# Optimization experiments

Hardware: AMD Instinct MI355X
Metric: run time of the kernel (lower is better)

Reference implementation:

```python
import jax, jax.numpy as jnp
import numpy as np

B, C, H, W = 4, 512, 128, 128
CI = C // 2   # inter_planes
CQ = C // 8   # q/k dim in CrossAttention


def conv1x1(x, w, b=None):
    # x: [B,Cin,H,W], w: [Cout,Cin]
    y = jnp.einsum('oc,bchw->bohw', w, x)
    if b is not None:
        y = y + b[None, :, None, None]
    return y


def setup_inputs() -> dict:
    key = jax.random.key(0)
    ks = jax.random.split(key, 13)
    s = 0.05
    return {
        'x': jax.random.normal(ks[0], (B, C, H, W), jnp.float32),
        # SCCA gating params (1x1 convs, no bias except conv_up)
        'w_q_right': jax.random.normal(ks[1], (1, C), jnp.float32) * s,
        'w_v_right': jax.random.normal(ks[2], (CI, C), jnp.float32) * s,
        'w_up': jax.random.normal(ks[3], (C, CI), jnp.float32) * s,
        'b_up': jnp.zeros((C,), jnp.float32),
        'w_q_left': jax.random.normal(ks[4], (CI, C), jnp.float32) * s,
        'w_v_left': jax.random.normal(ks[5], (CI, C), jnp.float32) * s,
        # CrossAttention params (1x1 convs with bias)
        'wq': jax.random.normal(ks[6], (CQ, C), jnp.float32) * s,
        'bq': jnp.zeros((CQ,), jnp.float32),
        'wk': jax.random.normal(ks[7], (CQ, C), jnp.float32) * s,
        'bk': jnp.zeros((CQ,), jnp.float32),
        'wv': jax.random.normal(ks[8], (C, C), jnp.float32) * s,
        'bv': jnp.zeros((C,), jnp.float32),
        'gamma': jnp.asarray(0.5, jnp.float32),
    }


def cross_attention(x, wq, bq, wk, bk, wv, bv, gamma):
    # criss-cross attention: each pixel attends to its row and column
    b, c, h, w = x.shape
    q = conv1x1(x, wq, bq)   # [B,CQ,H,W]
    k = conv1x1(x, wk, bk)   # [B,CQ,H,W]
    v = conv1x1(x, wv, bv)   # [B,C,H,W]
    # column (H) affinities with -inf on the self diagonal (as in INF())
    diag = jnp.where(jnp.eye(h, dtype=bool), -jnp.inf, 0.0).astype(x.dtype)
    e_h = jnp.einsum('bchw,bcgw->bhwg', q, k) + diag[None, :, None, :]  # [B,H,W,H]
    e_w = jnp.einsum('bchw,bchv->bhwv', q, k)                            # [B,H,W,W]
    att = jax.nn.softmax(jnp.concatenate([e_h, e_w], axis=-1), axis=-1)  # [B,H,W,H+W]
    a_h, a_w = att[..., :h], att[..., h:]
    out_h = jnp.einsum('bcgw,bhwg->bchw', v, a_h)
    out_w = jnp.einsum('bchv,bhwv->bchw', v, a_w)
    return gamma * (out_h + out_w) + x


def spatial_weighted(x, w_q_right, w_v_right, w_up, b_up):
    b, c, h, w = x.shape
    input_x = conv1x1(x, w_v_right).reshape(b, CI, h * w)       # [B,CI,HW]
    mask = jax.nn.softmax(conv1x1(x, w_q_right).reshape(b, h * w), axis=-1)  # [B,HW]
    ctx = jnp.einsum('bcn,bn->bc', input_x, mask)               # [B,CI]
    ctx = jnp.einsum('oc,bc->bo', w_up, ctx) + b_up             # [B,C]
    mask_ch = jax.nn.sigmoid(ctx)[:, :, None, None]
    return x * mask_ch


def channel_weighted(x, w_q_left, w_v_left):
    b, c, h, w = x.shape
    g_x = conv1x1(x, w_q_left)                                  # [B,CI,H,W]
    avg = g_x.mean(axis=(2, 3))                                 # [B,CI]
    theta = conv1x1(x, w_v_left).reshape(b, CI, h * w)          # [B,CI,HW]
    ctx = jax.nn.softmax(jnp.einsum('bc,bcn->bn', avg, theta), axis=-1)
    mask_sp = jax.nn.sigmoid(ctx).reshape(b, 1, h, w)
    return x * mask_sp


def reference(x, w_q_right, w_v_right, w_up, b_up, w_q_left, w_v_left,
              wq, bq, wk, bk, wv, bv, gamma):
    cc = spatial_weighted(x, w_q_right, w_v_right, w_up, b_up)
    cc = cross_attention(cc, wq, bq, wk, bk, wv, bv, gamma)
    cs = channel_weighted(x, w_q_left, w_v_left)
    cs = cross_attention(cs, wq, bq, wk, bk, wv, bv, gamma)
    out = cs + cc
    out = cross_attention(out, wq, bq, wk, bk, wv, bv, gamma)
    return out
```

## Files before the change

kernel.cpp:

```cpp
#include <hip/hip_runtime.h>
#include <hip/hip_bf16.h>
#include <math.h>

typedef __hip_bfloat16 bf16;
typedef __attribute__((ext_vector_type(8))) short s16x8;
typedef __attribute__((ext_vector_type(4))) float f32x4;

constexpr int Bn  = 4;
constexpr int Cn  = 512;
constexpr int Hn  = 128;
constexpr int Wn  = 128;
constexpr int Nn  = Hn * Wn;
constexpr int CQn = 64;
constexpr int CIn = 256;

__device__ __forceinline__ float bf2f(bf16 v){ return __bfloat162float(v); }
__device__ __forceinline__ bf16  f2bf(float v){ return __float2bfloat16(v); }

__device__ __forceinline__ void gload_lds16(const void* g, void* l){
  __builtin_amdgcn_global_load_lds(
      (const __attribute__((address_space(1))) unsigned int*)g,
      (__attribute__((address_space(3))) unsigned int*)l,
      16, 0, 0);
}


__global__ __launch_bounds__(256) void k_dotc(const float* __restrict__ x,
                                              const float* __restrict__ w,
                                              int wstride,
                                              float* __restrict__ out){
  int t = blockIdx.x * 256 + threadIdx.x;
  int b = t >> 14;
  const float* wp = w + (size_t)b * wstride;
  const float* xp = x + (size_t)b * Cn * Nn + (t & (Nn - 1));
  float acc = 0.f;
  #pragma unroll 8
  for (int c = 0; c < Cn; ++c) acc += wp[c] * xp[(size_t)c * Nn];
  out[t] = acc;
}

__global__ __launch_bounds__(256) void k_rowmean(const float* __restrict__ x,
                                                 float* __restrict__ out,
                                                 float scale){
  int bc = blockIdx.x;
  const float* xp = x + (size_t)bc * Nn;
  float acc = 0.f;
  for (int n = threadIdx.x; n < Nn; n += 256) acc += xp[n];
  for (int o = 32; o > 0; o >>= 1) acc += __shfl_down(acc, o);
  __shared__ float red[4];
  if ((threadIdx.x & 63) == 0) red[threadIdx.x >> 6] = acc;
  __syncthreads();
  if (threadIdx.x == 0) out[bc] = (red[0] + red[1] + red[2] + red[3]) * scale;
}

__global__ __launch_bounds__(256) void k_rowdot(const float* __restrict__ W,
                                                const float* __restrict__ vec,
                                                float* __restrict__ out){
  __shared__ float vs[Cn];
  int b = blockIdx.x, t = threadIdx.x;
  for (int j = t; j < Cn; j += 256) vs[j] = vec[b * Cn + j];
  __syncthreads();
  const float4* wp = (const float4*)(W + (size_t)t * Cn);
  float a = 0.f;
  #pragma unroll 4
  for (int j = 0; j < Cn / 4; ++j){
    float4 w4 = wp[j];
    a += w4.x * vs[4*j] + w4.y * vs[4*j+1] + w4.z * vs[4*j+2] + w4.w * vs[4*j+3];
  }
  out[b * CIn + t] = a;
}

__global__ __launch_bounds__(256) void k_coldot(const float* __restrict__ W,
                                                const float* __restrict__ vec,
                                                float* __restrict__ out){
  __shared__ float vs[CIn];
  int b = blockIdx.y, t = threadIdx.x;
  int c = blockIdx.x * 256 + t;
  if (t < CIn) vs[t] = vec[b * CIn + t];
  __syncthreads();
  float a = 0.f;
  #pragma unroll 8
  for (int j = 0; j < CIn; ++j) a += W[(size_t)j * Cn + c] * vs[j];
  out[b * Cn + c] = a;
}

__global__ __launch_bounds__(256) void k_mch2(const float* __restrict__ w_up,
                                              const float* __restrict__ b_up,
                                              const float* __restrict__ ctx,
                                              float* __restrict__ mch){
  __shared__ float cs[CIn];
  int b = blockIdx.y, t = threadIdx.x;
  int o = blockIdx.x * 256 + t;
  if (t < CIn) cs[t] = ctx[b * CIn + t];
  __syncthreads();
  const float4* wp = (const float4*)(w_up + (size_t)o * CIn);
  float a = b_up[o];
  #pragma unroll 4
  for (int j = 0; j < CIn / 4; ++j){
    float4 w4 = wp[j];
    a += w4.x * cs[4*j] + w4.y * cs[4*j+1] + w4.z * cs[4*j+2] + w4.w * cs[4*j+3];
  }
  mch[b * Cn + o] = 1.f / (1.f + expf(-a));
}

__global__ __launch_bounds__(1024) void k_stats(const float* __restrict__ vv,
                                                float* __restrict__ stats){
  int b = blockIdx.x;
  const float* pp = vv + (size_t)b * Nn;
  int t = threadIdx.x;
  float m = -3.4e38f;
  for (int n = t; n < Nn; n += 1024) m = fmaxf(m, pp[n]);
  for (int o = 32; o > 0; o >>= 1) m = fmaxf(m, __shfl_down(m, o));
  __shared__ float red[16];
  int wid = t >> 6, lid = t & 63;
  if (lid == 0) red[wid] = m;
  __syncthreads();
  if (t == 0){
    float q = red[0];
    for (int i = 1; i < 16; i++) q = fmaxf(q, red[i]);
    red[0] = q;
  }
  __syncthreads();
  m = red[0];
  __syncthreads();
  float s = 0.f;
  for (int n = t; n < Nn; n += 1024) s += expf(pp[n] - m);
  for (int o = 32; o > 0; o >>= 1) s += __shfl_down(s, o);
  if (lid == 0) red[wid] = s;
  __syncthreads();
  if (t == 0){
    float q = 0.f;
    for (int i = 0; i < 16; i++) q += red[i];
    stats[b * 2]     = m;
    stats[b * 2 + 1] = q;
  }
}

__global__ __launch_bounds__(256) void k_weighted(const float* __restrict__ x,
                                                  const float* __restrict__ logits,
                                                  const float* __restrict__ stats,
                                                  float* __restrict__ out){
  int bc = blockIdx.x;
  int b = bc >> 9;
  const float* xp = x + (size_t)bc * Nn;
  const float* lp = logits + (size_t)b * Nn;
  float m = stats[b * 2], den = stats[b * 2 + 1];
  float acc = 0.f;
  for (int n = threadIdx.x; n < Nn; n += 256) acc += xp[n] * expf(lp[n] - m);
  for (int o = 32; o > 0; o >>= 1) acc += __shfl_down(acc, o);
  __shared__ float red[4];
  if ((threadIdx.x & 63) == 0) red[threadIdx.x >> 6] = acc;
  __syncthreads();
  if (threadIdx.x == 0) out[bc] = (red[0] + red[1] + red[2] + red[3]) / den;
}

__global__ __launch_bounds__(256) void k_msp(const float* __restrict__ lg,
                                             const float* __restrict__ stats,
                                             float* __restrict__ msp){
  int t = blockIdx.x * 256 + threadIdx.x;
  int b = t >> 14;
  float v = expf(lg[t] - stats[b * 2]) / stats[b * 2 + 1];
  msp[t] = 1.f / (1.f + expf(-v));
}

__global__ __launch_bounds__(256) void k_applyT3(const float* __restrict__ x,
                                                 const float* __restrict__ mch,
                                                 const float* __restrict__ msp,
                                                 bf16* __restrict__ cc_hi,
                                                 bf16* __restrict__ cc_lo,
                                                 bf16* __restrict__ cs_hi,
                                                 bf16* __restrict__ cs_lo){
  __shared__ bf16 tch[32][33], tcl[32][33], tsh[32][33], tsl[32][33];
  int nt = blockIdx.x, ct = blockIdx.y, b = blockIdx.z;
  int n0 = nt * 32, c0 = ct * 32;
  int t = threadIdx.x;
  #pragma unroll
  for (int kk = 0; kk < 4; ++kk){
    int idx = t + kk * 256;
    int cl = idx >> 5, nl = idx & 31;
    float xv = x[((size_t)(b * Cn + c0 + cl)) * Nn + n0 + nl];
    float ccv = xv * mch[b * Cn + c0 + cl];
    float csv = xv * msp[b * Nn + n0 + nl];
    bf16 h1 = f2bf(ccv);
    tch[cl][nl] = h1;
    tcl[cl][nl] = f2bf(ccv - bf2f(h1));
    bf16 h2 = f2bf(csv);
    tsh[cl][nl] = h2;
    tsl[cl][nl] = f2bf(csv - bf2f(h2));
  }
  __syncthreads();
  #pragma unroll
  for (int kk = 0; kk < 4; ++kk){
    int idx = t + kk * 256;
    int nl = idx >> 5, cl = idx & 31;
    size_t o = ((size_t)(b * Nn + n0 + nl)) * Cn + c0 + cl;
    cc_hi[o] = tch[cl][nl];
    cc_lo[o] = tcl[cl][nl];
    cs_hi[o] = tsh[cl][nl];
    cs_lo[o] = tsl[cl][nl];
  }
}


__global__ __launch_bounds__(256) void k_cvt_w(const float* __restrict__ in,
                                               bf16* __restrict__ out, int n){
  int t = blockIdx.x * 256 + threadIdx.x;
  if (t < n) out[t] = f2bf(in[t]);
}

__global__ __launch_bounds__(256) void k_prep_wqk(const float* __restrict__ wq,
                                                  const float* __restrict__ wk,
                                                  const float* __restrict__ bq,
                                                  const float* __restrict__ bk,
                                                  bf16* __restrict__ wqk_hi,
                                                  bf16* __restrict__ wqk_lo,
                                                  float* __restrict__ bqk){
  int t = blockIdx.x * 256 + threadIdx.x;
  int o = t >> 9, c = t & 511;
  float v = (o < 64) ? wq[(size_t)o * Cn + c] : wk[(size_t)(o - 64) * Cn + c];
  bf16 h = f2bf(v);
  wqk_hi[t] = h;
  wqk_lo[t] = f2bf(v - bf2f(h));
  if (t < 128) bqk[t] = (t < 64) ? bq[t] : bk[t - 64];
}

__global__ __launch_bounds__(256) void k_cvt_T(const float* __restrict__ in,
                                               bf16* __restrict__ out_hi,
                                               bf16* __restrict__ out_lo){
  __shared__ bf16 th_[32][33];
  __shared__ bf16 tl_[32][33];
  int nt = blockIdx.x, ct = blockIdx.y, b = blockIdx.z;
  int n0 = nt * 32, c0 = ct * 32;
  int t = threadIdx.x;
  #pragma unroll
  for (int kk = 0; kk < 4; ++kk){
    int idx = t + kk * 256;
    int cl = idx >> 5, nl = idx & 31;
    float v = in[((size_t)(b * Cn + c0 + cl)) * Nn + n0 + nl];
    bf16 h = f2bf(v);
    th_[cl][nl] = h;
    tl_[cl][nl] = f2bf(v - bf2f(h));
  }
  __syncthreads();
  #pragma unroll
  for (int kk = 0; kk < 4; ++kk){
    int idx = t + kk * 256;
    int nl = idx >> 5, cl = idx & 31;
    size_t o = ((size_t)(b * Nn + n0 + nl)) * Cn + c0 + cl;
    out_hi[o] = th_[cl][nl];
    out_lo[o] = tl_[cl][nl];
  }
}


__global__ __launch_bounds__(256) void k_v_mfma(const bf16* __restrict__ xT,
                                                const bf16* __restrict__ wvb,
                                                const float* __restrict__ bv,
                                                bf16* __restrict__ v){
  __shared__ short As[128 * 64];
  __shared__ short Bs[128 * 64];
  __shared__ float bvs[128];
  int lin = blockIdx.x;
  int swz = (lin & 7) * 256 + (lin >> 3);
  int cb = (swz & 3) * 128;
  int nb = ((swz >> 2) & 127) * 128;
  int b  = swz >> 9;
  int t = threadIdx.x, lane = t & 63, wid = t >> 6;
  int wm = wid >> 1, wn = wid & 1;
  int l15 = lane & 15, l4 = lane >> 4;
  if (t < 128) bvs[t] = bv[cb + t];
  f32x4 acc[4][4];
  #pragma unroll
  for (int i = 0; i < 4; i++)
    #pragma unroll
    for (int j = 0; j < 4; j++) acc[i][j] = (f32x4){0.f, 0.f, 0.f, 0.f};

  const bf16* wp = wvb + (size_t)cb * Cn;
  const bf16* xp = xT + ((size_t)b * Nn + nb) * Cn;
  int r8 = lane >> 3;
  int kc = (lane & 7) * 8;
  for (int kt = 0; kt < 8; ++kt){
    int k0 = kt * 64;
    #pragma unroll
    for (int j = 0; j < 4; ++j){
      int inst = wid * 4 + j;
      int row = inst * 8 + r8;
      gload_lds16(wp + (size_t)row * Cn + k0 + kc, (char*)As + inst * 1024);
      gload_lds16(xp + (size_t)row * Cn + k0 + kc, (char*)Bs + inst * 1024);
    }
    __syncthreads();
    #pragma unroll
    for (int kk = 0; kk < 64; kk += 32){
      s16x8 a[4], bb[4];
      #pragma unroll
      for (int mi = 0; mi < 4; mi++)
        a[mi] = *(const s16x8*)&As[(wm * 64 + mi * 16 + l15) * 64 + kk + l4 * 8];
      #pragma unroll
      for (int ni = 0; ni < 4; ni++)
        bb[ni] = *(const s16x8*)&Bs[(wn * 64 + ni * 16 + l15) * 64 + kk + l4 * 8];
      #pragma unroll
      for (int mi = 0; mi < 4; mi++)
        #pragma unroll
        for (int ni = 0; ni < 4; ni++)
          acc[mi][ni] = __builtin_amdgcn_mfma_f32_16x16x32_bf16(a[mi], bb[ni], acc[mi][ni], 0, 0, 0);
    }
    __syncthreads();
  }
  #pragma unroll
  for (int mi = 0; mi < 4; mi++){
    #pragma unroll
    for (int r = 0; r < 4; r++){
      int cl = wm * 64 + mi * 16 + l4 * 4 + r;
      int c  = cb + cl;
      float bias = bvs[cl];
      #pragma unroll
      for (int ni = 0; ni < 4; ni++){
        int n = nb + wn * 64 + ni * 16 + l15;
        v[((size_t)(b * Cn + c)) * Nn + n] = f2bf(acc[mi][ni][r] + bias);
      }
    }
  }
}

__global__ __launch_bounds__(256) void k_qk_mfma(const bf16* __restrict__ xT_hi,
                                                 const bf16* __restrict__ xT_lo,
                                                 const bf16* __restrict__ wqk_hi,
                                                 const bf16* __restrict__ wqk_lo,
                                                 const float* __restrict__ bqk,
                                                 bf16* __restrict__ qhw,
                                                 bf16* __restrict__ khw){
  __shared__ char smem[65536];
  short* Ah = (short*)smem;
  short* Al = Ah + 8192;
  short* Bh = Al + 8192;
  short* Bl = Bh + 8192;
  char*  Os = smem;
  __shared__ float bs[128];
  int h = blockIdx.x, b = blockIdx.y;
  int nb = h * 128;
  int t = threadIdx.x, lane = t & 63, wid = t >> 6;
  int wm = wid >> 1, wn = wid & 1;
  int l15 = lane & 15, l4 = lane >> 4;
  if (t < 128) bs[t] = bqk[t];
  f32x4 acc[4][4];
  #pragma unroll
  for (int i = 0; i < 4; i++)
    #pragma unroll
    for (int j = 0; j < 4; j++) acc[i][j] = (f32x4){0.f, 0.f, 0.f, 0.f};

  const bf16* xh = xT_hi + ((size_t)b * Nn + nb) * Cn;
  const bf16* xl = xT_lo + ((size_t)b * Nn + nb) * Cn;
  int r8 = lane >> 3;
  int kc = (lane & 7) * 8;
  for (int kt = 0; kt < 8; ++kt){
    int k0 = kt * 64;
    #pragma unroll
    for (int j = 0; j < 4; ++j){
      int inst = wid * 4 + j;
      int row = inst * 8 + r8;
      size_t off = (size_t)row * Cn + k0 + kc;
      gload_lds16(wqk_hi + off, (char*)Ah + inst * 1024);
      gload_lds16(wqk_lo + off, (char*)Al + inst * 1024);
      gload_lds16(xh + off,     (char*)Bh + inst * 1024);
      gload_lds16(xl + off,     (char*)Bl + inst * 1024);
    }
    __syncthreads();
    #pragma unroll
    for (int kk = 0; kk < 64; kk += 32){
      s16x8 ah[4], al[4], bh[4], bl[4];
      #pragma unroll
      for (int mi = 0; mi < 4; mi++){
        int idx = (wm * 64 + mi * 16 + l15) * 64 + kk + l4 * 8;
        ah[mi] = *(const s16x8*)&Ah[idx];
        al[mi] = *(const s16x8*)&Al[idx];
      }
      #pragma unroll
      for (int ni = 0; ni < 4; ni++){
        int idx = (wn * 64 + ni * 16 + l15) * 64 + kk + l4 * 8;
        bh[ni] = *(const s16x8*)&Bh[idx];
        bl[ni] = *(const s16x8*)&Bl[idx];
      }
      #pragma unroll
      for (int mi = 0; mi < 4; mi++)
        #pragma unroll
        for (int ni = 0; ni < 4; ni++){
          acc[mi][ni] = __builtin_amdgcn_mfma_f32_16x16x32_bf16(ah[mi], bh[ni], acc[mi][ni], 0, 0, 0);
          acc[mi][ni] = __builtin_amdgcn_mfma_f32_16x16x32_bf16(ah[mi], bl[ni], acc[mi][ni], 0, 0, 0);
          acc[mi][ni] = __builtin_amdgcn_mfma_f32_16x16x32_bf16(al[mi], bh[ni], acc[mi][ni], 0, 0, 0);
        }
    }
    __syncthreads();
  }
  #pragma unroll
  for (int mi = 0; mi < 4; mi++){
    #pragma unroll
    for (int r = 0; r < 4; r++){
      int o = wm * 64 + mi * 16 + l4 * 4 + r;
      float bias = bs[o];
      #pragma unroll
      for (int ni = 0; ni < 4; ni++){
        int n = wn * 64 + ni * 16 + l15;
        bf16 bv = f2bf(acc[mi][ni][r] + bias);
        int byte = (n * 256 + o * 2) ^ ((n & 7) << 4);
        *(unsigned short*)(Os + byte) = *(unsigned short*)&bv;
      }
    }
  }
  __syncthreads();
  #pragma unroll
  for (int i = 0; i < 8; ++i){
    int s = t + i * 256;
    int row = s >> 3, seg = s & 7;
    int w = row & 127, qk = row >> 7;
    int o0 = qk * 64 + seg * 8;
    int byte = (w * 256 + o0 * 2) ^ ((w & 7) << 4);
    s16x8 d = *(const s16x8*)(Os + byte);
    bf16* dst = (qk == 0 ? qhw : khw) + (((size_t)b * Wn + w) * Hn + h) * CQn + seg * 8;
    *(s16x8*)dst = d;
  }
}


__global__ __launch_bounds__(256) void k_att_h(const bf16* __restrict__ qhw,
                                               const bf16* __restrict__ khw,
                                               const bf16* __restrict__ vT,
                                               float* __restrict__ mh,
                                               float* __restrict__ sh,
                                               bf16* __restrict__ ohX){
  __shared__ char smem[65536];
  char* attb = smem;
  char* vbb  = smem + 32768;
  float* redm = (float*)(smem + 32768);
  float* reds = redm + 256;
  int w = blockIdx.x, b = blockIdx.y;
  int t = threadIdx.x, lane = t & 63, wid = t >> 6;
  int wm = wid >> 1, wn = wid & 1;
  int l15 = lane & 15, l4 = lane >> 4;

  const bf16* qp = qhw + ((size_t)(b * Wn + w)) * (Hn * CQn);
  const bf16* kp = khw + ((size_t)(b * Wn + w)) * (Hn * CQn);
  f32x4 acc[4][4];
  #pragma unroll
  for (int i = 0; i < 4; i++)
    #pragma unroll
    for (int j = 0; j < 4; j++) acc[i][j] = (f32x4){0.f, 0.f, 0.f, 0.f};
  #pragma unroll
  for (int kk = 0; kk < 64; kk += 32){
    s16x8 a[4], bb[4];
    #pragma unroll
    for (int mi = 0; mi < 4; mi++)
      a[mi] = *(const s16x8*)(qp + (size_t)(wm * 64 + mi * 16 + l15) * CQn + kk + l4 * 8);
    #pragma unroll
    for (int ni = 0; ni < 4; ni++)
      bb[ni] = *(const s16x8*)(kp + (size_t)(wn * 64 + ni * 16 + l15) * CQn + kk + l4 * 8);
    #pragma unroll
    for (int mi = 0; mi < 4; mi++)
      #pragma unroll
      for (int ni = 0; ni < 4; ni++)
        acc[mi][ni] = __builtin_amdgcn_mfma_f32_16x16x32_bf16(a[mi], bb[ni], acc[mi][ni], 0, 0, 0);
  }
  if (wm == wn){
    #pragma unroll
    for (int mi = 0; mi < 4; mi++)
      #pragma unroll
      for (int r = 0; r < 4; r++)
        if (l15 == l4 * 4 + r) acc[mi][mi][r] = -1e30f;
  }
  float rm[4][4];
  #pragma unroll
  for (int mi = 0; mi < 4; mi++)
    #pragma unroll
    for (int r = 0; r < 4; r++){
      float m = fmaxf(fmaxf(acc[mi][0][r], acc[mi][1][r]),
                      fmaxf(acc[mi][2][r], acc[mi][3][r]));
      m = fmaxf(m, __shfl_xor(m, 1));
      m = fmaxf(m, __shfl_xor(m, 2));
      m = fmaxf(m, __shfl_xor(m, 4));
      m = fmaxf(m, __shfl_xor(m, 8));
      rm[mi][r] = m;
    }
  if (l15 == 0){
    #pragma unroll
    for (int mi = 0; mi < 4; mi++)
      #pragma unroll
      for (int r = 0; r < 4; r++)
        redm[wn * 128 + wm * 64 + mi * 16 + l4 * 4 + r] = rm[mi][r];
  }
  __syncthreads();
  float rs[4][4];
  #pragma unroll
  for (int mi = 0; mi < 4; mi++)
    #pragma unroll
    for (int r = 0; r < 4; r++){
      int h = wm * 64 + mi * 16 + l4 * 4 + r;
      float m = fmaxf(redm[h], redm[128 + h]);
      rm[mi][r] = m;
      float s = 0.f;
      #pragma unroll
      for (int ni = 0; ni < 4; ni++){
        acc[mi][ni][r] = expf(acc[mi][ni][r] - m);
        s += acc[mi][ni][r];
      }
      s += __shfl_xor(s, 1);
      s += __shfl_xor(s, 2);
      s += __shfl_xor(s, 4);
      s += __shfl_xor(s, 8);
      rs[mi][r] = s;
    }
  if (l15 == 0){
    #pragma unroll
    for (int mi = 0; mi < 4; mi++)
      #pragma unroll
      for (int r = 0; r < 4; r++)
        reds[wn * 128 + wm * 64 + mi * 16 + l4 * 4 + r] = rs[mi][r];
  }
  __syncthreads();
  #pragma unroll
  for (int mi = 0; mi < 4; mi++)
    #pragma unroll
    for (int r = 0; r < 4; r++){
      int h = wm * 64 + mi * 16 + l4 * 4 + r;
      if (wn == 0 && l15 == 0){
        mh[(size_t)(b * Wn + w) * Hn + h] = rm[mi][r];
        sh[(size_t)(b * Wn + w) * Hn + h] = reds[h] + reds[128 + h];
      }
      #pragma unroll
      for (int ni = 0; ni < 4; ni++){
        int g = wn * 64 + ni * 16 + l15;
        bf16 bv = f2bf(acc[mi][ni][r]);
        int byte = (h * 256 + g * 2) ^ ((h & 7) << 4);
        *(unsigned short*)(attb + byte) = *(unsigned short*)&bv;
      }
    }
  __syncthreads();
  for (int cb = 0; cb < Cn; cb += 128){
    const bf16* vp = vT + ((size_t)(b * Wn + w) * Cn + cb) * Hn;
    for (int s = t; s < 2048; s += 256){
      int row = s >> 4, seg = s & 15;
      s16x8 d = *(const s16x8*)(vp + (size_t)row * Hn + seg * 8);
      int byte = (row * 256 + seg * 16) ^ ((row & 7) << 4);
      *(s16x8*)(vbb + byte) = d;
    }
    __syncthreads();
    f32x4 acc2[4][4];
    #pragma unroll
    for (int i = 0; i < 4; i++)
      #pragma unroll
      for (int j = 0; j < 4; j++) acc2[i][j] = (f32x4){0.f, 0.f, 0.f, 0.f};
    #pragma unroll
    for (int kk = 0; kk < 128; kk += 32){
      s16x8 a[4], bb[4];
      #pragma unroll
      for (int mi = 0; mi < 4; mi++){
        int row = wm * 64 + mi * 16 + l15;
        int byte = (row * 256 + (kk + l4 * 8) * 2) ^ ((row & 7) << 4);
        a[mi] = *(const s16x8*)(vbb + byte);
      }
      #pragma unroll
      for (int ni = 0; ni < 4; ni++){
        int row = wn * 64 + ni * 16 + l15;
        int byte = (row * 256 + (kk + l4 * 8) * 2) ^ ((row & 7) << 4);
        bb[ni] = *(const s16x8*)(attb + byte);
      }
      #pragma unroll
      for (int mi = 0; mi < 4; mi++)
        #pragma unroll
        for (int ni = 0; ni < 4; ni++)
          acc2[mi][ni] = __builtin_amdgcn_mfma_f32_16x16x32_bf16(a[mi], bb[ni], acc2[mi][ni], 0, 0, 0);
    }
    bf16* op = ohX + ((size_t)(b * Cn + cb)) * Nn + (size_t)w * Hn;
    #pragma unroll
    for (int mi = 0; mi < 4; mi++)
      #pragma unroll
      for (int r = 0; r < 4; r++){
        int cl = wm * 64 + mi * 16 + l4 * 4 + r;
        #pragma unroll
        for (int ni = 0; ni < 4; ni++){
          int h = wn * 64 + ni * 16 + l15;
          op[(size_t)cl * Nn + h] = f2bf(acc2[mi][ni][r]);
        }
      }
    __syncthreads();
  }
}

__global__ __launch_bounds__(256) void k_att_w(const bf16* __restrict__ qhw,
                                               const bf16* __restrict__ khw,
                                               const bf16* __restrict__ v,
                                               float* __restrict__ mw,
                                               float* __restrict__ sw,
                                               bf16* __restrict__ ow){
  __shared__ char smem[65536];
  char* attb = smem;
  char* vbb  = smem + 32768;
  float* redm = (float*)(smem + 32768);
  float* reds = redm + 256;
  int h = blockIdx.x, b = blockIdx.y;
  int t = threadIdx.x, lane = t & 63, wid = t >> 6;
  int wm = wid >> 1, wn = wid & 1;
  int l15 = lane & 15, l4 = lane >> 4;

  const bf16* qp = qhw + (size_t)b * Wn * Hn * CQn + (size_t)h * CQn;
  const bf16* kp = khw + (size_t)b * Wn * Hn * CQn + (size_t)h * CQn;
  f32x4 acc[4][4];
  #pragma unroll
  for (int i = 0; i < 4; i++)
    #pragma unroll
    for (int j = 0; j < 4; j++) acc[i][j] = (f32x4){0.f, 0.f, 0.f, 0.f};
  #pragma unroll
  for (int kk = 0; kk < 64; kk += 32){
    s16x8 a[4], bb[4];
    #pragma unroll
    for (int mi = 0; mi < 4; mi++)
      a[mi] = *(const s16x8*)(qp + (size_t)(wm * 64 + mi * 16 + l15) * (Hn * CQn) + kk + l4 * 8);
    #pragma unroll
    for (int ni = 0; ni < 4; ni++)
      bb[ni] = *(const s16x8*)(kp + (size_t)(wn * 64 + ni * 16 + l15) * (Hn * CQn) + kk + l4 * 8);
    #pragma unroll
    for (int mi = 0; mi < 4; mi++)
      #pragma unroll
      for (int ni = 0; ni < 4; ni++)
        acc[mi][ni] = __builtin_amdgcn_mfma_f32_16x16x32_bf16(a[mi], bb[ni], acc[mi][ni], 0, 0, 0);
  }
  float rm[4][4];
  #pragma unroll
  for (int mi = 0; mi < 4; mi++)
    #pragma unroll
    for (int r = 0; r < 4; r++){
      float m = fmaxf(fmaxf(acc[mi][0][r], acc[mi][1][r]),
                      fmaxf(acc[mi][2][r], acc[mi][3][r]));
      m = fmaxf(m, __shfl_xor(m, 1));
      m = fmaxf(m, __shfl_xor(m, 2));
      m = fmaxf(m, __shfl_xor(m, 4));
      m = fmaxf(m, __shfl_xor(m, 8));
      rm[mi][r] = m;
    }
  if (l15 == 0){
    #pragma unroll
    for (int mi = 0; mi < 4; mi++)
      #pragma unroll
      for (int r = 0; r < 4; r++)
        redm[wn * 128 + wm * 64 + mi * 16 + l4 * 4 + r] = rm[mi][r];
  }
  __syncthreads();
  float rs[4][4];
  #pragma unroll
  for (int mi = 0; mi < 4; mi++)
    #pragma unroll
    for (int r = 0; r < 4; r++){
      int wr = wm * 64 + mi * 16 + l4 * 4 + r;
      float m = fmaxf(redm[wr], redm[128 + wr]);
      rm[mi][r] = m;
      float s = 0.f;
      #pragma unroll
      for (int ni = 0; ni < 4; ni++){
        acc[mi][ni][r] = expf(acc[mi][ni][r] - m);
        s += acc[mi][ni][r];
      }
      s += __shfl_xor(s, 1);
      s += __shfl_xor(s, 2);
      s += __shfl_xor(s, 4);
      s += __shfl_xor(s, 8);
      rs[mi][r] = s;
    }
  if (l15 == 0){
    #pragma unroll
    for (int mi = 0; mi < 4; mi++)
      #pragma unroll
      for (int r = 0; r < 4; r++)
        reds[wn * 128 + wm * 64 + mi * 16 + l4 * 4 + r] = rs[mi][r];
  }
  __syncthreads();
  #pragma unroll
  for (int mi = 0; mi < 4; mi++)
    #pragma unroll
    for (int r = 0; r < 4; r++){
      int wr = wm * 64 + mi * 16 + l4 * 4 + r;
      if (wn == 0 && l15 == 0){
        mw[(size_t)(b * Hn + h) * Wn + wr] = rm[mi][r];
        sw[(size_t)(b * Hn + h) * Wn + wr] = reds[wr] + reds[128 + wr];
      }
      #pragma unroll
      for (int ni = 0; ni < 4; ni++){
        int g = wn * 64 + ni * 16 + l15;
        bf16 bv = f2bf(acc[mi][ni][r]);
        int byte = (wr * 256 + g * 2) ^ ((wr & 7) << 4);
        *(unsigned short*)(attb + byte) = *(unsigned short*)&bv;
      }
    }
  __syncthreads();
  for (int cb = 0; cb < Cn; cb += 128){
    const bf16* vp = v + (size_t)(b * Cn + cb) * Nn + (size_t)h * Wn;
    for (int s = t; s < 2048; s += 256){
      int row = s >> 4, seg = s & 15;
      s16x8 d = *(const s16x8*)(vp + (size_t)row * Nn + seg * 8);
      int byte = (row * 256 + seg * 16) ^ ((row & 7) << 4);
      *(s16x8*)(vbb + byte) = d;
    }
    __syncthreads();
    f32x4 acc2[4][4];
    #pragma unroll
    for (int i = 0; i < 4; i++)
      #pragma unroll
      for (int j = 0; j < 4; j++) acc2[i][j] = (f32x4){0.f, 0.f, 0.f, 0.f};
    #pragma unroll
    for (int kk = 0; kk < 128; kk += 32){
      s16x8 a[4], bb[4];
      #pragma unroll
      for (int mi = 0; mi < 4; mi++){
        int row = wm * 64 + mi * 16 + l15;
        int byte = (row * 256 + (kk + l4 * 8) * 2) ^ ((row & 7) << 4);
        a[mi] = *(const s16x8*)(vbb + byte);
      }
      #pragma unroll
      for (int ni = 0; ni < 4; ni++){
        int row = wn * 64 + ni * 16 + l15;
        int byte = (row * 256 + (kk + l4 * 8) * 2) ^ ((row & 7) << 4);
        bb[ni] = *(const s16x8*)(attb + byte);
      }
      #pragma unroll
      for (int mi = 0; mi < 4; mi++)
        #pragma unroll
        for (int ni = 0; ni < 4; ni++)
          acc2[mi][ni] = __builtin_amdgcn_mfma_f32_16x16x32_bf16(a[mi], bb[ni], acc2[mi][ni], 0, 0, 0);
    }
    bf16* op = ow + (size_t)(b * Cn + cb) * Nn + (size_t)h * Wn;
    #pragma unroll
    for (int mi = 0; mi < 4; mi++)
      #pragma unroll
      for (int r = 0; r < 4; r++){
        int cl = wm * 64 + mi * 16 + l4 * 4 + r;
        #pragma unroll
        for (int ni = 0; ni < 4; ni++){
          int wr = wn * 64 + ni * 16 + l15;
          op[(size_t)cl * Nn + wr] = f2bf(acc2[mi][ni][r]);
        }
      }
    __syncthreads();
  }
}

__global__ __launch_bounds__(256) void k_alpha(const float* __restrict__ mh,
                                               const float* __restrict__ sh,
                                               const float* __restrict__ mw,
                                               const float* __restrict__ sw,
                                               float* __restrict__ ahT,
                                               float* __restrict__ aw){
  int t = blockIdx.x * 256 + threadIdx.x;
  int b = t >> 14;
  int hw = t & (Nn - 1);
  int h = hw >> 7, w = hw & 127;
  size_t ih = (size_t)(b * Wn + w) * Hn + h;
  size_t iw = t;
  float mhv = mh[ih], mwv = mw[iw];
  float M = fmaxf(mhv, mwv);
  float eh_ = expf(mhv - M), ew_ = expf(mwv - M);
  float inv = 1.f / (sh[ih] * eh_ + sw[iw] * ew_);
  ahT[t] = eh_ * inv;
  aw[t]  = ew_ * inv;
}


__global__ __launch_bounds__(256) void k_trans(const bf16* __restrict__ in,
                                               bf16* __restrict__ out,
                                               int CH){
  __shared__ bf16 tile[32][33];
  int tl = blockIdx.x, c = blockIdx.y, b = blockIdx.z;
  int th = tl >> 2, tw = tl & 3;
  int h0 = th * 32, w0 = tw * 32;
  int t = threadIdx.x;
  const bf16* ip = in + ((size_t)(b * CH + c)) * Nn;
  #pragma unroll
  for (int kk = 0; kk < 4; ++kk){
    int idx = t + kk * 256;
    int hl = idx >> 5, wl = idx & 31;
    tile[hl][wl] = ip[(h0 + hl) * Wn + w0 + wl];
  }
  __syncthreads();
  #pragma unroll
  for (int kk = 0; kk < 4; ++kk){
    int idx = t + kk * 256;
    int wl = idx >> 5, hl = idx & 31;
    out[((size_t)(b * Wn + w0 + wl) * CH + c) * Hn + h0 + hl] = tile[hl][wl];
  }
}

__global__ __launch_bounds__(256) void k_fuse2(const float* __restrict__ in,
                                               const bf16* __restrict__ ohX,
                                               const bf16* __restrict__ ow,
                                               const float* __restrict__ ahT,
                                               const float* __restrict__ aw,
                                               const float* __restrict__ gamma,
                                               float* __restrict__ out){
  __shared__ unsigned short tileT[64][138];
  int c = blockIdx.x, half = blockIdx.y, b = blockIdx.z;
  int t = threadIdx.x;
  float g = gamma[0];
  int h0 = half * 64;
  const bf16* ohp = ohX + ((size_t)(b * Cn + c)) * Nn;
  #pragma unroll
  for (int i = 0; i < 4; ++i){
    int s = t + i * 256;
    int w = s >> 3, seg = s & 7;
    s16x8 d = *(const s16x8*)(ohp + (size_t)w * Hn + h0 + seg * 8);
    #pragma unroll
    for (int j = 0; j < 8; ++j)
      tileT[seg * 8 + j][w] = (unsigned short)d[j];
  }
  __syncthreads();
  size_t base = ((size_t)(b * Cn + c)) * Nn;
  #pragma unroll
  for (int i = 0; i < 8; ++i){
    int o = t + i * 256;
    int hl = o >> 5, w4 = (o & 31) * 4;
    int h = h0 + hl;
    size_t idx = base + (size_t)h * Wn + w4;
    size_t aidx = (size_t)b * Nn + (size_t)h * Wn + w4;
    ushort4 owv = *(const ushort4*)((const unsigned short*)ow + idx);
    float4 ah4 = *(const float4*)(ahT + aidx);
    float4 aw4 = *(const float4*)(aw + aidx);
    float4 inv = in ? *(const float4*)(in + idx) : (float4){0.f,0.f,0.f,0.f};
    float r[4];
    #pragma unroll
    for (int j = 0; j < 4; ++j){
      unsigned short uh = tileT[hl][w4 + j];
      unsigned short uo = ((const unsigned short*)&owv)[j];
      float ohv = bf2f(*(bf16*)&uh);
      float owf = bf2f(*(bf16*)&uo);
      float ahv = ((const float*)&ah4)[j];
      float awv = ((const float*)&aw4)[j];
      r[j] = g * (ahv * ohv + awv * owf) + ((const float*)&inv)[j];
    }
    float4 o4 = { r[0], r[1], r[2], r[3] };
    *(float4*)(out + idx) = o4;
  }
}

__global__ __launch_bounds__(256) void k_fuse3(const float* __restrict__ x,
                                               const float* __restrict__ mch,
                                               const float* __restrict__ msp,
                                               const bf16* __restrict__ oh1,
                                               const bf16* __restrict__ ow1,
                                               const float* __restrict__ a1h,
                                               const float* __restrict__ a1w,
                                               const bf16* __restrict__ oh2,
                                               const bf16* __restrict__ ow2,
                                               const float* __restrict__ a2h,
                                               const float* __restrict__ a2w,
                                               const float* __restrict__ gamma,
                                               float* __restrict__ out){
  __shared__ unsigned short t1[64][138];
  __shared__ unsigned short t2[64][138];
  int c = blockIdx.x, half = blockIdx.y, b = blockIdx.z;
  int t = threadIdx.x;
  float g = gamma[0];
  float mc = mch[b * Cn + c];
  int h0 = half * 64;
  const bf16* p1 = oh1 + ((size_t)(b * Cn + c)) * Nn;
  const bf16* p2 = oh2 + ((size_t)(b * Cn + c)) * Nn;
  #pragma unroll
  for (int i = 0; i < 4; ++i){
    int s = t + i * 256;
    int w = s >> 3, seg = s & 7;
    s16x8 d1 = *(const s16x8*)(p1 + (size_t)w * Hn + h0 + seg * 8);
    s16x8 d2 = *(const s16x8*)(p2 + (size_t)w * Hn + h0 + seg * 8);
    #pragma unroll
    for (int j = 0; j < 8; ++j){
      t1[seg * 8 + j][w] = (unsigned short)d1[j];
      t2[seg * 8 + j][w] = (unsigned short)d2[j];
    }
  }
  __syncthreads();
  size_t base = ((size_t)(b * Cn + c)) * Nn;
  #pragma unroll
  for (int i = 0; i < 8; ++i){
    int o = t + i * 256;
    int hl = o >> 5, w4 = (o & 31) * 4;
    int h = h0 + hl;
    size_t idx = base + (size_t)h * Wn + w4;
    size_t aidx = (size_t)b * Nn + (size_t)h * Wn + w4;
    ushort4 o1v = *(const ushort4*)((const unsigned short*)ow1 + idx);
    ushort4 o2v = *(const ushort4*)((const unsigned short*)ow2 + idx);
    float4 a1h4 = *(const float4*)(a1h + aidx);
    float4 a1w4 = *(const float4*)(a1w + aidx);
    float4 a2h4 = *(const float4*)(a2h + aidx);
    float4 a2w4 = *(const float4*)(a2w + aidx);
    float4 xv4  = *(const float4*)(x + idx);
    float4 mn4  = *(const float4*)(msp + aidx);
    float r[4];
    #pragma unroll
    for (int j = 0; j < 4; ++j){
      unsigned short u1 = t1[hl][w4 + j];
      unsigned short u2 = t2[hl][w4 + j];
      unsigned short w1 = ((const unsigned short*)&o1v)[j];
      unsigned short w2 = ((const unsigned short*)&o2v)[j];
      float oh1v = bf2f(*(bf16*)&u1), ow1v = bf2f(*(bf16*)&w1);
      float oh2v = bf2f(*(bf16*)&u2), ow2v = bf2f(*(bf16*)&w2);
      float term1 = g * (((const float*)&a1h4)[j] * oh1v + ((const float*)&a1w4)[j] * ow1v);
      float term2 = g * (((const float*)&a2h4)[j] * oh2v + ((const float*)&a2w4)[j] * ow2v);
      float resid = ((const float*)&xv4)[j] * (mc + ((const float*)&mn4)[j]);
      r[j] = term2 + resid + term1;
    }
    float4 o4 = { r[0], r[1], r[2], r[3] };
    *(float4*)(out + idx) = o4;
  }
}


static void run_att(const bf16* xT_hi, const bf16* xT_lo,
                    const bf16* wqk_hi, const bf16* wqk_lo, const float* bqk,
                    const bf16* wvb, const float* bv,
                    bf16* qhw, bf16* khw, bf16* v, bf16* vT,
                    float* mh, float* sh, float* mw, float* sw,
                    float* ahT, float* aw, bf16* tmp, hipStream_t stream){
  bf16* ohX = tmp;
  bf16* ow  = tmp + (size_t)Bn * Cn * Nn;
  k_qk_mfma<<<dim3(Nn / 128, Bn), 256, 0, stream>>>(xT_hi, xT_lo, wqk_hi, wqk_lo, bqk,
                                                    qhw, khw);
  k_v_mfma<<<2048, 256, 0, stream>>>(xT_hi, wvb, bv, v);
  k_trans<<<dim3(16, Cn, Bn), 256, 0, stream>>>(v, vT, Cn);
  k_att_h<<<dim3(Wn, Bn), 256, 0, stream>>>(qhw, khw, vT, mh, sh, ohX);
  k_att_w<<<dim3(Hn, Bn), 256, 0, stream>>>(qhw, khw, v, mw, sw, ow);
  k_alpha<<<Bn * Nn / 256, 256, 0, stream>>>(mh, sh, mw, sw, ahT, aw);
}

extern "C" void kernel_launch(void* const* d_in, const int* in_sizes, int n_in,
                              void* d_out, int out_size, void* d_ws, size_t ws_size,
                              hipStream_t stream){
  (void)in_sizes; (void)n_in; (void)out_size; (void)ws_size;
  const float* x         = (const float*)d_in[0];
  const float* w_q_right = (const float*)d_in[1];
  const float* w_v_right = (const float*)d_in[2];
  const float* w_up      = (const float*)d_in[3];
  const float* b_up      = (const float*)d_in[4];
  const float* w_q_left  = (const float*)d_in[5];
  const float* w_v_left  = (const float*)d_in[6];
  const float* wq        = (const float*)d_in[7];
  const float* bq        = (const float*)d_in[8];
  const float* wk        = (const float*)d_in[9];
  const float* bk        = (const float*)d_in[10];
  const float* wv        = (const float*)d_in[11];
  const float* bv        = (const float*)d_in[12];
  const float* gamma     = (const float*)d_in[13];

  const size_t SZ_MAP = (size_t)Bn * Cn * Nn;
  char* p = (char*)d_ws;
  float* buf0   = (float*)p; p += SZ_MAP * 4;
  float* buf1   = (float*)p; p += SZ_MAP * 4;
  bf16*  vbuf   = (bf16*)p;  p += SZ_MAP * 2;
  bf16*  vT     = (bf16*)p;  p += SZ_MAP * 2;
  bf16*  qhw    = (bf16*)p;  p += (size_t)Bn * CQn * Nn * 2;
  bf16*  khw    = (bf16*)p;  p += (size_t)Bn * CQn * Nn * 2;
  float* ebuf   = (float*)p; p += (size_t)SZ_MAP * 2;
  float* logits = (float*)p; p += (size_t)Bn * Nn * 4;
  float* ctxlog = (float*)p; p += (size_t)Bn * Nn * 4;
  float* msp    = (float*)p; p += (size_t)Bn * Nn * 4;
  float* xbar   = (float*)p; p += Bn * Cn * 4;
  float* wgt    = (float*)p; p += Bn * Cn * 4;
  float* u      = (float*)p; p += Bn * Cn * 4;
  float* mch    = (float*)p; p += Bn * Cn * 4;
  float* avg    = (float*)p; p += Bn * CIn * 4;
  float* ctx    = (float*)p; p += Bn * CIn * 4;
  float* stats_sp = (float*)p; p += 64;
  float* stats_ch = (float*)p; p += 64;
  bf16*  wvb    = (bf16*)p;  p += (size_t)Cn * Cn * 2;
  bf16*  wqk_hi = (bf16*)p;  p += (size_t)128 * Cn * 2;
  bf16*  wqk_lo = (bf16*)p;  p += (size_t)128 * Cn * 2;
  float* bqk    = (float*)p; p += 128 * 4;
  float* mh     = (float*)p; p += (size_t)Bn * Nn * 4;
  float* sh     = (float*)p; p += (size_t)Bn * Nn * 4;
  float* mw     = (float*)p; p += (size_t)Bn * Nn * 4;
  float* sw     = (float*)p; p += (size_t)Bn * Nn * 4;
  float* ah1    = (float*)p; p += (size_t)Bn * Nn * 4;
  float* aw1    = (float*)p; p += (size_t)Bn * Nn * 4;
  float* ah2    = (float*)p; p += (size_t)Bn * Nn * 4;
  float* aw2    = (float*)p; p += (size_t)Bn * Nn * 4;

  bf16*  cc_hi  = (bf16*)ebuf;
  bf16*  cc_lo  = (bf16*)d_out;
  bf16*  cs_hi  = (bf16*)buf1;
  bf16*  cs_lo  = (bf16*)buf1 + SZ_MAP;
  bf16*  xT_hi3 = (bf16*)ebuf;
  bf16*  xT_lo3 = (bf16*)d_out;

  k_cvt_w<<<(Cn * Cn + 255) / 256, 256, 0, stream>>>(wv, wvb, Cn * Cn);
  k_prep_wqk<<<(128 * Cn) / 256, 256, 0, stream>>>(wq, wk, bq, bk, wqk_hi, wqk_lo, bqk);

  k_dotc<<<Bn * Nn / 256, 256, 0, stream>>>(x, w_q_right, 0, logits);
  k_rowmean<<<Bn * Cn, 256, 0, stream>>>(x, xbar, 1.f / Nn);
  k_rowdot<<<Bn, 256, 0, stream>>>(w_q_left, xbar, avg);
  k_coldot<<<dim3(Cn / 256, Bn), 256, 0, stream>>>(w_v_left, avg, u);
  k_stats<<<Bn, 1024, 0, stream>>>(logits, stats_sp);
  k_weighted<<<Bn * Cn, 256, 0, stream>>>(x, logits, stats_sp, wgt);
  k_rowdot<<<Bn, 256, 0, stream>>>(w_v_right, wgt, ctx);
  k_mch2<<<dim3(Cn / 256, Bn), 256, 0, stream>>>(w_up, b_up, ctx, mch);
  k_dotc<<<Bn * Nn / 256, 256, 0, stream>>>(x, u, Cn, ctxlog);
  k_stats<<<Bn, 1024, 0, stream>>>(ctxlog, stats_ch);
  k_msp<<<Bn * Nn / 256, 256, 0, stream>>>(ctxlog, stats_ch, msp);

  k_applyT3<<<dim3(Nn / 32, Cn / 32, Bn), 256, 0, stream>>>(x, mch, msp,
                                                            cc_hi, cc_lo, cs_hi, cs_lo);

  run_att(cc_hi, cc_lo, wqk_hi, wqk_lo, bqk, wvb, bv,
          qhw, khw, vbuf, vT, mh, sh, mw, sw, ah1, aw1, (bf16*)d_out, stream);
  run_att(cs_hi, cs_lo, wqk_hi, wqk_lo, bqk, wvb, bv,
          qhw, khw, vbuf, vT, mh, sh, mw, sw, ah2, aw2, (bf16*)buf0, stream);
  k_fuse3<<<dim3(Cn, 2, Bn), 256, 0, stream>>>(x, mch, msp,
                                               (const bf16*)d_out,
                                               (const bf16*)d_out + SZ_MAP, ah1, aw1,
                                               (const bf16*)buf0,
                                               (const bf16*)buf0 + SZ_MAP, ah2, aw2,
                                               gamma, buf1);
  k_cvt_T<<<dim3(Nn / 32, Cn / 32, Bn), 256, 0, stream>>>(buf1, xT_hi3, xT_lo3);
  run_att(xT_hi3, xT_lo3, wqk_hi, wqk_lo, bqk, wvb, bv,
          qhw, khw, vbuf, vT, mh, sh, mw, sw, ah1, aw1, (bf16*)buf0, stream);
  k_fuse2<<<dim3(Cn, 2, Bn), 256, 0, stream>>>(buf1, (const bf16*)buf0,
                                               (const bf16*)buf0 + SZ_MAP, ah1, aw1,
                                               gamma, (float*)d_out);
}
```

Before: 1.274 ms.

## Fuse gating reductions into two passes over x with partial sums

Replaces four separate full passes over x (logit dot, per-channel mean, weighted channel sum, context logit dot) with two fused passes. Each pass computes a per-pixel dot product while also reducing x per channel with wavefront shuffles into per-block partial sums. Small follow-up kernels then reduce the partials. This cuts global reads of the 128MB input from four passes to two. The cost is a six-step shuffle reduction per channel per element, plus a partial-sum buffer.

Measured after the change: 1.698 ms. 1.33x slower.

```diff
diff --git a/kernel.cpp b/kernel.cpp
--- a/kernel.cpp
+++ b/kernel.cpp
@@ -25,32 +25,89 @@
 }
 
 
-__global__ __launch_bounds__(256) void k_dotc(const float* __restrict__ x,
-                                              const float* __restrict__ w,
-                                              int wstride,
-                                              float* __restrict__ out){
-  int t = blockIdx.x * 256 + threadIdx.x;
-  int b = t >> 14;
-  const float* wp = w + (size_t)b * wstride;
-  const float* xp = x + (size_t)b * Cn * Nn + (t & (Nn - 1));
+__global__ __launch_bounds__(256) void k_pass1(const float* __restrict__ x,
+                                               const float* __restrict__ wqr,
+                                               float* __restrict__ logits,
+                                               float* __restrict__ pxb){
+  __shared__ float xbw[4][Cn];
+  int blk = blockIdx.x, b = blockIdx.y;
+  int t = threadIdx.x, wid = t >> 6;
+  int n = blk * 256 + t;
+  const float* xp = x + (size_t)b * Cn * Nn + n;
   float acc = 0.f;
+  #pragma unroll 4
+  for (int c = 0; c < Cn; ++c){
+    float xv = xp[(size_t)c * Nn];
+    acc += wqr[c] * xv;
+    float s = xv;
+    s += __shfl_xor(s, 1);
+    s += __shfl_xor(s, 2);
+    s += __shfl_xor(s, 4);
+    s += __shfl_xor(s, 8);
+    s += __shfl_xor(s, 16);
+    s += __shfl_xor(s, 32);
+    if ((t & 63) == 0) xbw[wid][c] = s;
+  }
+  logits[b * Nn + n] = acc;
+  __syncthreads();
+  for (int c = t; c < Cn; c += 256)
+    pxb[((size_t)b * 64 + blk) * Cn + c] = xbw[0][c] + xbw[1][c] + xbw[2][c] + xbw[3][c];
+}
+
+__global__ __launch_bounds__(256) void k_red1(const float* __restrict__ pxb,
+                                              float* __restrict__ xbar,
+                                              float scale){
+  int i = blockIdx.x * 256 + threadIdx.x;
+  int b = i >> 9, c = i & 511;
+  float s = 0.f;
   #pragma unroll 8
-  for (int c = 0; c < Cn; ++c) acc += wp[c] * xp[(size_t)c * Nn];
-  out[t] = acc;
-}
-
-__global__ __launch_bounds__(256) void k_rowmean(const float* __restrict__ x,
-                                                 float* __restrict__ out,
-                                                 float scale){
-  int bc = blockIdx.x;
-  const float* xp = x + (size_t)bc * Nn;
+  for (int k = 0; k < 64; ++k) s += pxb[((size_t)b * 64 + k) * Cn + c];
+  xbar[i] = s * scale;
+}
+
+__global__ __launch_bounds__(256) void k_pass2(const float* __restrict__ x,
+                                               const float* __restrict__ u,
+                                               const float* __restrict__ logits,
+                                               const float* __restrict__ stats,
+                                               float* __restrict__ ctxlog,
+                                               float* __restrict__ pwg){
+  __shared__ float xbw[4][Cn];
+  int blk = blockIdx.x, b = blockIdx.y;
+  int t = threadIdx.x, wid = t >> 6;
+  int n = blk * 256 + t;
+  float m = stats[b * 2];
+  float we = expf(logits[b * Nn + n] - m);
+  const float* xp = x + (size_t)b * Cn * Nn + n;
+  const float* up = u + b * Cn;
   float acc = 0.f;
-  for (int n = threadIdx.x; n < Nn; n += 256) acc += xp[n];
-  for (int o = 32; o > 0; o >>= 1) acc += __shfl_down(acc, o);
-  __shared__ float red[4];
-  if ((threadIdx.x & 63) == 0) red[threadIdx.x >> 6] = acc;
-  __syncthreads();
-  if (threadIdx.x == 0) out[bc] = (red[0] + red[1] + red[2] + red[3]) * scale;
+  #pragma unroll 4
+  for (int c = 0; c < Cn; ++c){
+    float xv = xp[(size_t)c * Nn];
+    acc += up[c] * xv;
+    float s = xv * we;
+    s += __shfl_xor(s, 1);
+    s += __shfl_xor(s, 2);
+    s += __shfl_xor(s, 4);
+    s += __shfl_xor(s, 8);
+    s += __shfl_xor(s, 16);
+    s += __shfl_xor(s, 32);
+    if ((t & 63) == 0) xbw[wid][c] = s;
+  }
+  ctxlog[b * Nn + n] = acc;
+  __syncthreads();
+  for (int c = t; c < Cn; c += 256)
+    pwg[((size_t)b * 64 + blk) * Cn + c] = xbw[0][c] + xbw[1][c] + xbw[2][c] + xbw[3][c];
+}
+
+__global__ __launch_bounds__(256) void k_red2(const float* __restrict__ pwg,
+                                              const float* __restrict__ stats,
+                                              float* __restrict__ wgt){
+  int i = blockIdx.x * 256 + threadIdx.x;
+  int b = i >> 9, c = i & 511;
+  float s = 0.f;
+  #pragma unroll 8
+  for (int k = 0; k < 64; ++k) s += pwg[((size_t)b * 64 + k) * Cn + c];
+  wgt[i] = s / stats[b * 2 + 1];
 }
 
 __global__ __launch_bounds__(256) void k_rowdot(const float* __restrict__ W,
@@ -134,24 +191,6 @@
     stats[b * 2]     = m;
     stats[b * 2 + 1] = q;
   }
-}
-
-__global__ __launch_bounds__(256) void k_weighted(const float* __restrict__ x,
-                                                  const float* __restrict__ logits,
-                                                  const float* __restrict__ stats,
-                                                  float* __restrict__ out){
-  int bc = blockIdx.x;
-  int b = bc >> 9;
-  const float* xp = x + (size_t)bc * Nn;
-  const float* lp = logits + (size_t)b * Nn;
-  float m = stats[b * 2], den = stats[b * 2 + 1];
-  float acc = 0.f;
-  for (int n = threadIdx.x; n < Nn; n += 256) acc += xp[n] * expf(lp[n] - m);
-  for (int o = 32; o > 0; o >>= 1) acc += __shfl_down(acc, o);
-  __shared__ float red[4];
-  if ((threadIdx.x & 63) == 0) red[threadIdx.x >> 6] = acc;
-  __syncthreads();
-  if (threadIdx.x == 0) out[bc] = (red[0] + red[1] + red[2] + red[3]) / den;
 }
 
 __global__ __launch_bounds__(256) void k_msp(const float* __restrict__ lg,
@@ -975,6 +1014,7 @@
   float* aw1    = (float*)p; p += (size_t)Bn * Nn * 4;
   float* ah2    = (float*)p; p += (size_t)Bn * Nn * 4;
   float* aw2    = (float*)p; p += (size_t)Bn * Nn * 4;
+  float* pxb    = (float*)p; p += (size_t)Bn * 64 * Cn * 4;
 
   bf16*  cc_hi  = (bf16*)ebuf;
   bf16*  cc_lo  = (bf16*)d_out;
@@ -986,16 +1026,16 @@
   k_cvt_w<<<(Cn * Cn + 255) / 256, 256, 0, stream>>>(wv, wvb, Cn * Cn);
   k_prep_wqk<<<(128 * Cn) / 256, 256, 0, stream>>>(wq, wk, bq, bk, wqk_hi, wqk_lo, bqk);
 
-  k_dotc<<<Bn * Nn / 256, 256, 0, stream>>>(x, w_q_right, 0, logits);
-  k_rowmean<<<Bn * Cn, 256, 0, stream>>>(x, xbar, 1.f / Nn);
+  k_pass1<<<dim3(Nn / 256, Bn), 256, 0, stream>>>(x, w_q_right, logits, pxb);
+  k_red1<<<Bn * Cn / 256, 256, 0, stream>>>(pxb, xbar, 1.f / Nn);
   k_rowdot<<<Bn, 256, 0, stream>>>(w_q_left, xbar, avg);
   k_coldot<<<dim3(Cn / 256, Bn), 256, 0, stream>>>(w_v_left, avg, u);
   k_stats<<<Bn, 1024, 0, stream>>>(logits, stats_sp);
-  k_weighted<<<Bn * Cn, 256, 0, stream>>>(x, logits, stats_sp, wgt);
+  k_pass2<<<dim3(Nn / 256, Bn), 256, 0, stream>>>(x, u, logits, stats_sp, ctxlog, pxb);
+  k_stats<<<Bn, 1024, 0, stream>>>(ctxlog, stats_ch);
+  k_red2<<<Bn * Cn / 256, 256, 0, stream>>>(pxb, stats_sp, wgt);
   k_rowdot<<<Bn, 256, 0, stream>>>(w_v_right, wgt, ctx);
   k_mch2<<<dim3(Cn / 256, Bn), 256, 0, stream>>>(w_up, b_up, ctx, mch);
-  k_dotc<<<Bn * Nn / 256, 256, 0, stream>>>(x, u, Cn, ctxlog);
-  k_stats<<<Bn, 1024, 0, stream>>>(ctxlog, stats_ch);
   k_msp<<<Bn * Nn / 256, 256, 0, stream>>>(ctxlog, stats_ch, msp);
 
   k_applyT3<<<dim3(Nn / 32, Cn / 32, Bn), 256, 0, stream>>>(x, mch, msp,
```
